# Performance work log

Hardware: AMD Instinct MI355X
Metric: run time of the kernel (lower is better)

Reference implementation:

```python
import math
import jax, jax.numpy as jnp
import numpy as np

HIDDEN = 2048
NUM_HEADS = 32
HEAD_DIM = HIDDEN // NUM_HEADS
NUM_BLOCKS = 4
INTER = 2 * HIDDEN
EPS = 1e-5
ROPE_THETA = 10000.0


def setup_inputs() -> dict:
    key = jax.random.key(0)
    ks = jax.random.split(key, 6)
    B, S = 2, 2048
    sc = 0.02
    return {
        "x": jax.random.normal(ks[0], (B, S, HIDDEN), jnp.float32),
        "attn_norm_w": jnp.ones((HIDDEN,), jnp.float32),
        "ffn_norm_w": jnp.ones((HIDDEN,), jnp.float32),
        "w_qkv": jax.random.normal(ks[1], (3 * HIDDEN, HIDDEN), jnp.float32) * sc,
        "w_o": jax.random.normal(ks[2], (HIDDEN, HIDDEN), jnp.float32) * sc,
        "w_up": jax.random.normal(ks[3], (2 * INTER, HIDDEN), jnp.float32) * sc,
        "w_down": jax.random.normal(ks[4], (HIDDEN, INTER), jnp.float32) * sc,
    }


def _rmsnorm(x, w):
    var = jnp.mean(x * x, axis=-1, keepdims=True)
    return x * jax.lax.rsqrt(var + EPS) * w


def _rope_cache(seq_len, dim, theta, scale):
    inv_freq = 1.0 / (theta ** (jnp.arange(0, dim, 2, dtype=jnp.float32) / dim))
    t = jnp.arange(seq_len, dtype=jnp.float32) / scale
    freqs = jnp.outer(t, inv_freq)                     # [S, D/2]
    emb = jnp.concatenate([freqs, freqs], axis=-1)     # [S, D]
    return jnp.cos(emb), jnp.sin(emb)


def _apply_rope(x, cos, sin):
    # x: [B, H, S, D]
    d2 = x.shape[-1] // 2
    x1, x2 = x[..., :d2], x[..., d2:]
    rot = jnp.concatenate([-x2, x1], axis=-1)
    return x * cos[None, None] + rot * sin[None, None]


def reference(x, attn_norm_w, ffn_norm_w, w_qkv, w_o, w_up, w_down):
    B, S, _ = x.shape
    residual = x
    h = _rmsnorm(x, attn_norm_w)

    qkv = jnp.einsum('bsh,oh->bso', h, w_qkv)
    qkv = qkv.reshape(B, S, 3, NUM_HEADS, HEAD_DIM)
    q, k, v = qkv[:, :, 0], qkv[:, :, 1], qkv[:, :, 2]
    q = q.transpose(0, 2, 1, 3)  # [B,H,S,D]
    k = k.transpose(0, 2, 1, 3)
    v = v.transpose(0, 2, 1, 3)

    cos, sin = _rope_cache(S, HEAD_DIM, ROPE_THETA, 1.0)
    q = _apply_rope(q, cos, sin)
    k = _apply_rope(k, cos, sin)

    scale = 1.0 / math.sqrt(HEAD_DIM)
    attn = jnp.einsum('bhqd,bhkd->bhqk', q, k) * scale

    num_blocks = max(1, min(NUM_BLOCKS, S))
    blk = math.ceil(S / num_blocks)
    pos = jnp.arange(S)
    block_ids = pos // blk
    block_mask = block_ids[:, None] != block_ids[None, :]
    causal_mask = pos[:, None] < pos[None, :]
    invalid = causal_mask | block_mask                 # [S,S]
    mask_floor = jnp.finfo(attn.dtype).min
    attn = jnp.where(invalid[None, None], mask_floor, attn)

    attn = jax.nn.softmax(attn, axis=-1)
    context = jnp.einsum('bhqk,bhkd->bhqd', attn, v)
    context = context.transpose(0, 2, 1, 3).reshape(B, S, HIDDEN)

    x = residual + jnp.einsum('bsh,oh->bso', context, w_o)

    residual = x
    h = _rmsnorm(x, ffn_norm_w)
    up = jnp.einsum('bsh,oh->bso', h, w_up)
    gate, value = up[..., :INTER], up[..., INTER:]
    down = jnp.einsum('bsi,oi->bso', jax.nn.silu(gate) * value, w_down)
    return residual + down
```

## Files before the change

kernel.cpp:

```cpp
#include <hip/hip_runtime.h>
#include <cstdint>
#include <cstddef>

typedef __bf16 bf16x8 __attribute__((ext_vector_type(8)));
typedef __bf16 bf16x4 __attribute__((ext_vector_type(4)));
typedef float  f32x4  __attribute__((ext_vector_type(4)));

#define TOKENS  4096
#define SEQLEN  2048
#define HID     2048
#define QKV_W   6144
#define UP_W    8192
#define INTER_  4096

__device__ __forceinline__ void async16(const void* g, void* l) {
  __builtin_amdgcn_global_load_lds(
      (__attribute__((address_space(1))) void*)(g),
      (__attribute__((address_space(3))) void*)(l), 16, 0, 0);
}

__global__ __launch_bounds__(256) void cvt_kernel(const float* __restrict__ src,
                                                  __bf16* __restrict__ dst, int n4) {
  int i = blockIdx.x * 256 + threadIdx.x;
  if (i >= n4) return;
  float4 f = ((const float4*)src)[i];
  bf16x4 o;
  o[0] = (__bf16)f.x; o[1] = (__bf16)f.y; o[2] = (__bf16)f.z; o[3] = (__bf16)f.w;
  ((bf16x4*)dst)[i] = o;
}

__global__ __launch_bounds__(256) void rmsnorm_kernel(const float* __restrict__ x,
                                                      const float* __restrict__ wgt,
                                                      __bf16* __restrict__ out) {
  const int tok = blockIdx.x;
  const int t = threadIdx.x;
  const float4* xr = (const float4*)(x + (long)tok * HID);
  float4 a = xr[t], b = xr[t + 256];
  float ss = a.x*a.x + a.y*a.y + a.z*a.z + a.w*a.w
           + b.x*b.x + b.y*b.y + b.z*b.z + b.w*b.w;
  #pragma unroll
  for (int off = 32; off; off >>= 1) ss += __shfl_xor(ss, off);
  __shared__ float red[4];
  if ((t & 63) == 0) red[t >> 6] = ss;
  __syncthreads();
  float tot = red[0] + red[1] + red[2] + red[3];
  float r = rsqrtf(tot * (1.0f / HID) + 1e-5f);
  const float4* wr = (const float4*)wgt;
  float4 wa = wr[t], wb = wr[t + 256];
  bf16x4 o0, o1;
  o0[0] = (__bf16)(a.x * r * wa.x); o0[1] = (__bf16)(a.y * r * wa.y);
  o0[2] = (__bf16)(a.z * r * wa.z); o0[3] = (__bf16)(a.w * r * wa.w);
  o1[0] = (__bf16)(b.x * r * wb.x); o1[1] = (__bf16)(b.y * r * wb.y);
  o1[2] = (__bf16)(b.z * r * wb.z); o1[3] = (__bf16)(b.w * r * wb.w);
  bf16x4* orow = (bf16x4*)(out + (long)tok * HID);
  orow[t] = o0; orow[t + 256] = o1;
}

template<bool OUT_BF16, bool ADD_RES, bool ROPE, bool SILU>
__global__ __launch_bounds__(256) void gemm_bt(const __bf16* __restrict__ A, int lda,
                                               const __bf16* __restrict__ B, int ldb,
                                               void* Cv, int ldc,
                                               const float* __restrict__ Res, int K) {
  __shared__ __align__(16) __bf16 As[128 * 64];
  __shared__ __align__(16) __bf16 Bs[128 * 64];
  const int t = threadIdx.x;
  const int lane = t & 63;
  const int w = t >> 6;
  const int wm = (w >> 1) * 64, wn = (w & 1) * 64;
  const int m0 = blockIdx.y * 128;
  const int n0 = SILU ? blockIdx.x * 64 : blockIdx.x * 128;
  const int sr = t >> 3;
  const int sc = (((t & 7) ^ (sr & 7)) * 8);
  const __bf16* Ag = A + (long)(m0 + sr) * lda + sc;
  const __bf16* Bg = B + (long)(n0 + sr) * ldb + sc;
  char* lA = (char*)As + t * 16;
  char* lB = (char*)Bs + t * 16;
  const int lr = lane & 15;
  const int lq = lane >> 4;
  f32x4 acc[4][4] = {};
  for (int k0 = 0; k0 < K; k0 += 64) {
    __syncthreads();
    #pragma unroll
    for (int c = 0; c < 4; c++)
      async16(Ag + (long)(c * 32) * lda + k0, lA + c * 4096);
    #pragma unroll
    for (int c = 0; c < 4; c++) {
      const long rowoff = SILU ? (long)((c & 1) * INTER_ + (c >> 1) * 32) * ldb
                               : (long)(c * 32) * ldb;
      async16(Bg + rowoff + k0, lB + c * 4096);
    }
    __syncthreads();
    #pragma unroll
    for (int ks = 0; ks < 2; ks++) {
      const int pos = (((ks * 4 + lq) ^ (lr & 7)) * 8);
      bf16x8 af[4], bfr[4];
      #pragma unroll
      for (int i = 0; i < 4; i++)
        af[i]  = *(const bf16x8*)(As + (wm + i * 16 + lr) * 64 + pos);
      #pragma unroll
      for (int j = 0; j < 4; j++)
        bfr[j] = *(const bf16x8*)(Bs + (wn + j * 16 + lr) * 64 + pos);
      #pragma unroll
      for (int i = 0; i < 4; i++)
        #pragma unroll
        for (int j = 0; j < 4; j++)
          acc[i][j] = __builtin_amdgcn_mfma_f32_16x16x32_bf16(af[i], bfr[j], acc[i][j], 0, 0, 0);
    }
  }
  const int lq4 = lq * 4;
  #pragma unroll
  for (int i = 0; i < 4; i++) {
    #pragma unroll
    for (int r = 0; r < 4; r++) {
      const long row = m0 + wm + i * 16 + lq4 + r;
      #pragma unroll
      for (int j = 0; j < 4; j++) {
        const long col = n0 + wn + j * 16 + lr;
        float v = acc[i][j][r];
        if (ADD_RES) v += Res[row * (long)ldc + col];
        if (OUT_BF16) ((__bf16*)Cv)[row * (long)ldc + col] = (__bf16)v;
        else          ((float*)Cv)[row * (long)ldc + col] = v;
      }
    }
  }
}

template<bool ROPE, bool SILU>
__global__ __launch_bounds__(512, 2) void gemm8p(const __bf16* __restrict__ A, int lda,
                                                 const __bf16* __restrict__ B, int ldb,
                                                 void* Cv, int ldc, int K) {
  __shared__ __align__(16) __bf16 As[2 * 16384];
  __shared__ __align__(16) __bf16 Bs[2 * 16384];
  const int tid  = threadIdx.x;
  const int lane = tid & 63;
  const int w    = tid >> 6;
  const int wm2  = w >> 2;
  const int wn4  = w & 3;
  const int lr   = lane & 15;
  const int lq   = lane >> 4;
  const int m0   = blockIdx.y * 256;
  const int n0   = ROPE ? blockIdx.x * 256 : 0;
  const int n0c  = SILU ? blockIdx.x * 128 : 0;

  const long r0 = tid >> 3;
  const int  e  = (((tid & 7) ^ ((int)r0 & 7)) * 8);
  const __bf16* Ap0 = A + (long)(m0 + r0) * lda + e;
  long br0, br1, bhs;
  if (ROPE) {
    br0 = n0 + 64 * (((int)r0 >> 5) & 3) + ((int)r0 & 31);
    br1 = n0 + 64 * ((((int)r0 + 64) >> 5) & 3) + ((int)r0 & 31);
    bhs = 32 * (long)ldb;
  } else {
    br0 = n0c + r0;
    br1 = n0c + r0 + 64;
    bhs = (long)INTER_ * ldb;
  }
  const __bf16* Bp0 = B + br0 * ldb + e;
  const __bf16* Bp1 = B + br1 * ldb + e;
  char* sA = (char*)As;
  char* sB = (char*)Bs;
  const int tid16 = tid * 16;

#define STAGE_A(h_, nb_, kk_) do {                                                     \
    async16(Ap0 + (long)((h_) * 128) * lda + (kk_),      sA + (nb_)*32768 + (h_)*16384 + tid16);        \
    async16(Ap0 + (long)((h_) * 128 + 64) * lda + (kk_), sA + (nb_)*32768 + (h_)*16384 + 8192 + tid16); \
  } while (0)
#define STAGE_B(h_, nb_, kk_) do {                                                     \
    async16(Bp0 + (h_) * bhs + (kk_), sB + (nb_)*32768 + (h_)*16384 + tid16);          \
    async16(Bp1 + (h_) * bhs + (kk_), sB + (nb_)*32768 + (h_)*16384 + 8192 + tid16);   \
  } while (0)

  const int ch0 = ((lq ^ (lr & 7)) * 16);
  const int ch1 = (((4 + lq) ^ (lr & 7)) * 16);
  const int abase = (wm2 * 64 + lr) * 128;
  const int bbase = (wn4 * 32 + lr) * 128;

  f32x4 acc[8][4] = {};
  bf16x8 af[4][2], bfr[4][2];
  const int NT = K >> 6;

#define LOAD_A(mh_) do {                                                               \
    _Pragma("unroll")                                                                  \
    for (int i = 0; i < 4; i++) {                                                      \
      af[i][0] = *(const bf16x8*)(Ab + abase + (mh_)*16384 + i*2048 + ch0);            \
      af[i][1] = *(const bf16x8*)(Ab + abase + (mh_)*16384 + i*2048 + ch1);            \
    } } while (0)
#define LOAD_B(nh_) do {                                                               \
    _Pragma("unroll")                                                                  \
    for (int j = 0; j < 2; j++) {                                                      \
      bfr[(nh_)*2 + j][0] = *(const bf16x8*)(Bb + bbase + (nh_)*16384 + j*2048 + ch0); \
      bfr[(nh_)*2 + j][1] = *(const bf16x8*)(Bb + bbase + (nh_)*16384 + j*2048 + ch1); \
    } } while (0)
#define MFMA_Q(mh_, nh_) do {                                                          \
    __builtin_amdgcn_s_setprio(1);                                                     \
    _Pragma("unroll")                                                                  \
    for (int ks = 0; ks < 2; ks++)                                                     \
      _Pragma("unroll")                                                                \
      for (int i = 0; i < 4; i++)                                                      \
        _Pragma("unroll")                                                              \
        for (int j = 0; j < 2; j++)                                                    \
          acc[(mh_)*4 + i][(nh_)*2 + j] = __builtin_amdgcn_mfma_f32_16x16x32_bf16(     \
              af[i][ks], bfr[(nh_)*2 + j][ks], acc[(mh_)*4 + i][(nh_)*2 + j], 0, 0, 0);\
    __builtin_amdgcn_s_setprio(0);                                                     \
  } while (0)
#define SBAR() do { __builtin_amdgcn_sched_barrier(0);                                 \
    __builtin_amdgcn_s_barrier(); __builtin_amdgcn_sched_barrier(0); } while (0)
#define LGKM0() do { asm volatile("s_waitcnt lgkmcnt(0)" ::: "memory");                \
    __builtin_amdgcn_sched_barrier(0); } while (0)

  STAGE_A(0, 0, 0); STAGE_B(0, 0, 0); STAGE_B(1, 0, 0); STAGE_A(1, 0, 0);
  asm volatile("s_waitcnt vmcnt(4)" ::: "memory");
  SBAR();

  for (int T = 0; T < NT; ++T) {
    const int cb = T & 1, nb = cb ^ 1;
    const int kk = (T + 1) << 6;
    const bool st = (T + 1 < NT);
    const char* Ab = (const char*)As + cb * 32768;
    const char* Bb = (const char*)Bs + cb * 32768;
    LOAD_A(0); LOAD_B(0);
    if (st) { STAGE_A(0, nb, kk); STAGE_B(0, nb, kk); }
    SBAR(); LGKM0();
    MFMA_Q(0, 0);
    if (st) asm volatile("s_waitcnt vmcnt(6)" ::: "memory");
    else    asm volatile("s_waitcnt vmcnt(2)" ::: "memory");
    SBAR();
    LOAD_B(1);
    if (st) STAGE_B(1, nb, kk);
    SBAR(); LGKM0();
    MFMA_Q(0, 1);
    if (st) asm volatile("s_waitcnt vmcnt(6)" ::: "memory");
    else    asm volatile("s_waitcnt vmcnt(0)" ::: "memory");
    SBAR();
    LOAD_A(1);
    if (st) STAGE_A(1, nb, kk);
    SBAR(); LGKM0();
    MFMA_Q(1, 0);
    SBAR();
    MFMA_Q(1, 1);
    if (st) asm volatile("s_waitcnt vmcnt(4)" ::: "memory");
    SBAR();
  }
#undef STAGE_A
#undef STAGE_B
#undef LOAD_A
#undef LOAD_B
#undef MFMA_Q
#undef SBAR
#undef LGKM0

  const int lq4 = lq * 4;
  if (ROPE) {
    if (n0 < 4096) {
      const float invf0 = exp2f((float)(lr)      * -0.41524101186092029f);
      const float invf1 = exp2f((float)(16 + lr) * -0.41524101186092029f);
      #pragma unroll
      for (int mi = 0; mi < 8; mi++) {
        #pragma unroll
        for (int r = 0; r < 4; r++) {
          const long row = m0 + (mi >> 2) * 128 + wm2 * 64 + (mi & 3) * 16 + lq4 + r;
          const float s = (float)(int)(row & (SEQLEN - 1));
          __bf16* crow = (__bf16*)Cv + row * (long)ldc + n0 + wn4 * 64 + lr;
          #pragma unroll
          for (int nj = 0; nj < 2; nj++) {
            float x1 = acc[mi][nj][r], x2 = acc[mi][nj + 2][r];
            float ang = s * (nj ? invf1 : invf0);
            float sn, cs;
            __sincosf(ang, &sn, &cs);
            crow[nj * 16]      = (__bf16)(x1 * cs - x2 * sn);
            crow[nj * 16 + 32] = (__bf16)(x2 * cs + x1 * sn);
          }
        }
      }
    } else {
      #pragma unroll
      for (int mi = 0; mi < 8; mi++) {
        #pragma unroll
        for (int r = 0; r < 4; r++) {
          const long row = m0 + (mi >> 2) * 128 + wm2 * 64 + (mi & 3) * 16 + lq4 + r;
          __bf16* crow = (__bf16*)Cv + row * (long)ldc + n0 + wn4 * 64 + lr;
          #pragma unroll
          for (int njf = 0; njf < 4; njf++)
            crow[(njf >> 1) * 32 + (njf & 1) * 16] = (__bf16)acc[mi][njf][r];
        }
      }
    }
  } else {
    #pragma unroll
    for (int mi = 0; mi < 8; mi++) {
      #pragma unroll
      for (int r = 0; r < 4; r++) {
        const long row = m0 + (mi >> 2) * 128 + wm2 * 64 + (mi & 3) * 16 + lq4 + r;
        #pragma unroll
        for (int nj = 0; nj < 2; nj++) {
          const long col = n0c + wn4 * 32 + nj * 16 + lr;
          float g = acc[mi][nj][r];
          float v = acc[mi][nj + 2][r];
          float sg = g / (1.0f + __expf(-g));
          ((__bf16*)Cv)[row * (long)ldc + col] = (__bf16)(sg * v);
        }
      }
    }
  }
}

__global__ __launch_bounds__(256) void attn_kernel(const __bf16* __restrict__ qkv,
                                                   __bf16* __restrict__ ctx) {
  const int qt   = blockIdx.x;
  const int head = blockIdx.y;
  const int b    = blockIdx.z;
  const int w    = threadIdx.x >> 6;
  const int lane = threadIdx.x & 63;
  const int lr = lane & 15;
  const int lq = lane >> 4;
  const int q0   = qt * 64;
  const int blk0 = q0 & ~511;
  const int nkv  = q0 + 64 - blk0;
  const int NT   = nkv >> 5;
  const long tok0 = (long)b * SEQLEN;

  const int qrow = q0 + w * 16 + lr;
  const long qoff = (tok0 + qrow) * QKV_W + head * 64 + lq * 8;
  bf16x8 qf0 = *(const bf16x8*)(qkv + qoff);
  bf16x8 qf1 = *(const bf16x8*)(qkv + qoff + 32);

  __shared__ __align__(16) char VTb[8192];
  __shared__ __align__(16) char Pbb[8192];

  const __bf16* kp = qkv + (tok0 + blk0 + lr) * QKV_W + HID + head * 64 + lq * 8;
  const int skv = threadIdx.x & 31;
  const int sd0 = (threadIdx.x >> 5) * 8;
  const __bf16* vp = qkv + (tok0 + blk0 + skv) * QKV_W + 2 * HID + head * 64 + sd0;

  bf16x8 ka[2][2], kb[2][2];

#define LOADK(KN, tk) do { \
    KN[0][0] = *(const bf16x8*)(kp + (long)(tk) * QKV_W); \
    KN[0][1] = *(const bf16x8*)(kp + (long)(tk) * QKV_W + 32); \
    KN[1][0] = *(const bf16x8*)(kp + (long)((tk) + 16) * QKV_W); \
    KN[1][1] = *(const bf16x8*)(kp + (long)((tk) + 16) * QKV_W + 32); \
  } while (0)

#define WRITEV(vr_, hb_) do { \
    const int c_ = (hb_) * 4 + (skv >> 3); \
    char* vb_ = VTb + sd0 * 128 + ((skv & 7) * 2); \
    _Pragma("unroll") \
    for (int i_ = 0; i_ < 8; i_++) \
      *(__bf16*)(vb_ + i_ * 128 + ((c_ ^ i_) * 16)) = vr_[i_]; \
  } while (0)

  LOADK(ka, 0);
  {
    bf16x8 vr0 = *(const bf16x8*)(vp);
    WRITEV(vr0, 0);
  }
  __syncthreads();

  float m[4], l[4];
  f32x4 oacc[4] = {};
  #pragma unroll
  for (int r = 0; r < 4; r++) { m[r] = -1e30f; l[r] = 0.0f; }
  const int myrow = q0 + w * 16 + lq * 4;

#define ITER(t_, hb_, KC, KN) { \
    const int tkn_ = ((t_) + 1) * 32; \
    const bool more_ = ((t_) + 1 < NT); \
    bf16x8 vr_ = {}; \
    if (more_) { LOADK(KN, tkn_); vr_ = *(const bf16x8*)(vp + (long)tkn_ * QKV_W); } \
    f32x4 s0 = {0.f, 0.f, 0.f, 0.f}, s1 = {0.f, 0.f, 0.f, 0.f}; \
    s0 = __builtin_amdgcn_mfma_f32_16x16x32_bf16(qf0, KC[0][0], s0, 0, 0, 0); \
    s0 = __builtin_amdgcn_mfma_f32_16x16x32_bf16(qf1, KC[0][1], s0, 0, 0, 0); \
    s1 = __builtin_amdgcn_mfma_f32_16x16x32_bf16(qf0, KC[1][0], s1, 0, 0, 0); \
    s1 = __builtin_amdgcn_mfma_f32_16x16x32_bf16(qf1, KC[1][1], s1, 0, 0, 0); \
    const int kpos0_ = blk0 + (t_) * 32 + lr; \
    float p0[4], p1[4], alpha[4]; \
    _Pragma("unroll") \
    for (int r = 0; r < 4; r++) { \
      float v0 = s0[r] * 0.125f, v1 = s1[r] * 0.125f; \
      v0 = (kpos0_      <= myrow + r) ? v0 : -1e30f; \
      v1 = (kpos0_ + 16 <= myrow + r) ? v1 : -1e30f; \
      float mx = fmaxf(v0, v1); \
      mx = fmaxf(mx, __shfl_xor(mx, 1)); \
      mx = fmaxf(mx, __shfl_xor(mx, 2)); \
      mx = fmaxf(mx, __shfl_xor(mx, 4)); \
      mx = fmaxf(mx, __shfl_xor(mx, 8)); \
      float mn = fmaxf(m[r], mx); \
      alpha[r] = __expf(m[r] - mn); \
      m[r] = mn; \
      p0[r] = __expf(v0 - mn); \
      p1[r] = __expf(v1 - mn); \
      float rs = p0[r] + p1[r]; \
      rs += __shfl_xor(rs, 1); rs += __shfl_xor(rs, 2); \
      rs += __shfl_xor(rs, 4); rs += __shfl_xor(rs, 8); \
      l[r] = l[r] * alpha[r] + rs; \
    } \
    _Pragma("unroll") \
    for (int dt = 0; dt < 4; dt++) \
      _Pragma("unroll") \
      for (int r = 0; r < 4; r++) oacc[dt][r] *= alpha[r]; \
    { \
      char* pw_ = Pbb + w * 2048 + (lq * 4) * 128 + ((lr & 7) * 2); \
      const int cl_ = (hb_) * 4 + (lr >> 3); \
      _Pragma("unroll") \
      for (int r = 0; r < 4; r++) { \
        const int q7_ = (lq * 4 + r) & 7; \
        *(__bf16*)(pw_ + r * 128 + (((cl_    ) ^ q7_) * 16)) = (__bf16)p0[r]; \
        *(__bf16*)(pw_ + r * 128 + (((cl_ + 2) ^ q7_) * 16)) = (__bf16)p1[r]; \
      } \
    } \
    asm volatile("s_waitcnt lgkmcnt(0)" ::: "memory"); \
    const int swz_ = (((hb_) * 4 + lq) ^ (lr & 7)) * 16; \
    bf16x8 pf_ = *(const bf16x8*)(Pbb + w * 2048 + lr * 128 + swz_); \
    _Pragma("unroll") \
    for (int dt = 0; dt < 4; dt++) { \
      bf16x8 vf_ = *(const bf16x8*)(VTb + dt * 2048 + lr * 128 + swz_); \
      oacc[dt] = __builtin_amdgcn_mfma_f32_16x16x32_bf16(pf_, vf_, oacc[dt], 0, 0, 0); \
    } \
    __syncthreads(); \
    if (more_) WRITEV(vr_, (hb_) ^ 1); \
    __syncthreads(); \
  }

  for (int t2 = 0; t2 < NT; t2 += 2) {
    ITER(t2, 0, ka, kb)
    ITER(t2 + 1, 1, kb, ka)
  }
#undef ITER
#undef LOADK
#undef WRITEV

  #pragma unroll
  for (int r = 0; r < 4; r++) {
    float inv = 1.0f / l[r];
    long obase = (tok0 + myrow + r) * HID + head * 64;
    #pragma unroll
    for (int dt = 0; dt < 4; dt++)
      ctx[obase + dt * 16 + lr] = (__bf16)(oacc[dt][r] * inv);
  }
}

extern "C" void kernel_launch(void* const* d_in, const int* in_sizes, int n_in,
                              void* d_out, int out_size, void* d_ws, size_t ws_size,
                              hipStream_t stream) {
  const float* x      = (const float*)d_in[0];
  const float* anw    = (const float*)d_in[1];
  const float* fnw    = (const float*)d_in[2];
  const float* w_qkv  = (const float*)d_in[3];
  const float* w_o    = (const float*)d_in[4];
  const float* w_up   = (const float*)d_in[5];
  const float* w_down = (const float*)d_in[6];
  float* out = (float*)d_out;

  char* wsb = (char*)d_ws;
  __bf16* ABUF = (__bf16*)wsb;
  __bf16* QKV  = (__bf16*)(wsb + (size_t)16777216);
  __bf16* WBUF = (__bf16*)(wsb + (size_t)83886080);
  __bf16* ACT  = QKV;

  rmsnorm_kernel<<<TOKENS, 256, 0, stream>>>(x, anw, ABUF);
  cvt_kernel<<<(QKV_W * HID / 4 + 255) / 256, 256, 0, stream>>>(w_qkv, WBUF, QKV_W * HID / 4);
  gemm8p<true, false><<<dim3(4096 / 256, TOKENS / 256), 512, 0, stream>>>(
      ABUF, HID, WBUF, HID, (void*)QKV, QKV_W, HID);
  gemm_bt<true, false, false, false><<<dim3(HID / 128, TOKENS / 128), 256, 0, stream>>>(
      ABUF, HID, WBUF + (size_t)4096 * HID, HID, (void*)(QKV + 4096), QKV_W, nullptr, HID);
  attn_kernel<<<dim3(SEQLEN / 64, 32, 2), 256, 0, stream>>>(QKV, ABUF);
  cvt_kernel<<<(HID * HID / 4 + 255) / 256, 256, 0, stream>>>(w_o, WBUF, HID * HID / 4);
  gemm_bt<false, true, false, false><<<dim3(HID / 128, TOKENS / 128), 256, 0, stream>>>(
      ABUF, HID, WBUF, HID, (void*)out, HID, x, HID);

  rmsnorm_kernel<<<TOKENS, 256, 0, stream>>>(out, fnw, ABUF);
  cvt_kernel<<<(UP_W * HID / 4 + 255) / 256, 256, 0, stream>>>(w_up, WBUF, UP_W * HID / 4);
  gemm8p<false, true><<<dim3(INTER_ / 128, TOKENS / 256), 512, 0, stream>>>(
      ABUF, HID, WBUF, HID, (void*)ACT, INTER_, HID);
  cvt_kernel<<<(HID * INTER_ / 4 + 255) / 256, 256, 0, stream>>>(w_down, WBUF, HID * INTER_ / 4);
  gemm_bt<false, true, false, false><<<dim3(HID / 128, TOKENS / 128), 256, 0, stream>>>(
      ACT, INTER_, WBUF, INTER_, (void*)out, HID, out, INTER_);
}
```

Baseline: 553.0 us.

## Add BK=32 specialized up-projection GEMM with SwiGLU epilogue and higher occupancy

Adds a dedicated kernel for the FFN up-projection that uses a K-tile of 32 with double-buffered async global-to-LDS loads. It also uses a swizzled LDS layout and a staged load/MFMA schedule with explicit waitcnts and barriers. The smaller LDS footprint and launch bounds of 4 blocks per CU aim to raise occupancy and overlap loads with MFMA work. In exchange it runs more loop iterations with more barriers per unit of K.

```diff
diff --git a/kernel.cpp b/kernel.cpp
--- a/kernel.cpp
+++ b/kernel.cpp
@@ -299,6 +299,124 @@
           float sg = g / (1.0f + __expf(-g));
           ((__bf16*)Cv)[row * (long)ldc + col] = (__bf16)(sg * v);
         }
+      }
+    }
+  }
+}
+
+__global__ __launch_bounds__(512, 4) void gemm_up32(const __bf16* __restrict__ A, int lda,
+                                                    const __bf16* __restrict__ B, int ldb,
+                                                    void* Cv, int ldc, int K) {
+  __shared__ __align__(16) __bf16 As[2 * 8192];
+  __shared__ __align__(16) __bf16 Bs[2 * 8192];
+  const int tid  = threadIdx.x;
+  const int lane = tid & 63;
+  const int w    = tid >> 6;
+  const int wm2  = w >> 2;
+  const int wn4  = w & 3;
+  const int lr   = lane & 15;
+  const int lq   = lane >> 4;
+  const int m0   = blockIdx.y * 256;
+  const int n0c  = blockIdx.x * 128;
+
+  const int sr = tid >> 2;
+  const int g8 = ((((tid & 3) - ((tid >> 3) & 3)) & 3) * 8);
+  const __bf16* ApS = A + (long)(m0 + sr) * lda + g8;
+  const __bf16* BpS = B + (long)(n0c + sr) * ldb + g8;
+  char* sA = (char*)As;
+  char* sB = (char*)Bs;
+  const int tid16 = tid * 16;
+
+#define STAGE_A32(h_, nb_, kk_) \
+    async16(ApS + (long)((h_) * 128) * lda + (kk_), sA + (nb_)*16384 + (h_)*8192 + tid16)
+#define STAGE_B32(h_, nb_, kk_) \
+    async16(BpS + (h_) * ((long)INTER_ * ldb) + (kk_), sB + (nb_)*16384 + (h_)*8192 + tid16)
+
+  const int p16   = ((lq + ((lr >> 1) & 3)) & 3) * 16;
+  const int abase = (wm2 * 64 + lr) * 64 + p16;
+  const int bbase = (wn4 * 32 + lr) * 64 + p16;
+
+  f32x4 acc[8][4] = {};
+  bf16x8 af[4], bfr[4];
+  const int NT = K >> 5;
+
+#define LOAD_A32(mh_, buf_) do {                                                       \
+    const char* p_ = sA + (buf_)*16384 + (mh_)*8192 + abase;                           \
+    _Pragma("unroll")                                                                  \
+    for (int i = 0; i < 4; i++) af[i] = *(const bf16x8*)(p_ + i * 1024);               \
+  } while (0)
+#define LOAD_B32(nh_, buf_) do {                                                       \
+    const char* p_ = sB + (buf_)*16384 + (nh_)*8192 + bbase;                           \
+    _Pragma("unroll")                                                                  \
+    for (int j = 0; j < 2; j++) bfr[(nh_)*2 + j] = *(const bf16x8*)(p_ + j * 1024);    \
+  } while (0)
+#define MFMA_Q32(mh_, nh_) do {                                                        \
+    __builtin_amdgcn_s_setprio(1);                                                     \
+    _Pragma("unroll")                                                                  \
+    for (int i = 0; i < 4; i++)                                                        \
+      _Pragma("unroll")                                                                \
+      for (int j = 0; j < 2; j++)                                                      \
+        acc[(mh_)*4 + i][(nh_)*2 + j] = __builtin_amdgcn_mfma_f32_16x16x32_bf16(       \
+            af[i], bfr[(nh_)*2 + j], acc[(mh_)*4 + i][(nh_)*2 + j], 0, 0, 0);          \
+    __builtin_amdgcn_s_setprio(0);                                                     \
+  } while (0)
+#define SBAR() do { __builtin_amdgcn_sched_barrier(0);                                 \
+    __builtin_amdgcn_s_barrier(); __builtin_amdgcn_sched_barrier(0); } while (0)
+#define LGKM0() do { asm volatile("s_waitcnt lgkmcnt(0)" ::: "memory");                \
+    __builtin_amdgcn_sched_barrier(0); } while (0)
+
+  STAGE_A32(0, 0, 0); STAGE_B32(0, 0, 0); STAGE_B32(1, 0, 0); STAGE_A32(1, 0, 0);
+  asm volatile("s_waitcnt vmcnt(1)" ::: "memory");
+  SBAR();
+
+  for (int T = 0; T < NT; ++T) {
+    const int cb = T & 1, nb = cb ^ 1;
+    const int kk = (T + 1) << 5;
+    const bool st = (T + 1 < NT);
+    LOAD_A32(0, cb); LOAD_B32(0, cb);
+    if (st) { STAGE_A32(0, nb, kk); STAGE_B32(0, nb, kk); }
+    SBAR(); LGKM0();
+    MFMA_Q32(0, 0);
+    if (st) asm volatile("s_waitcnt vmcnt(3)" ::: "memory");
+    else    asm volatile("s_waitcnt vmcnt(1)" ::: "memory");
+    SBAR();
+    LOAD_B32(1, cb);
+    if (st) STAGE_B32(1, nb, kk);
+    SBAR(); LGKM0();
+    MFMA_Q32(0, 1);
+    if (st) asm volatile("s_waitcnt vmcnt(3)" ::: "memory");
+    else    asm volatile("s_waitcnt vmcnt(0)" ::: "memory");
+    SBAR();
+    LOAD_A32(1, cb);
+    if (st) STAGE_A32(1, nb, kk);
+    SBAR(); LGKM0();
+    MFMA_Q32(1, 0);
+    SBAR();
+    MFMA_Q32(1, 1);
+    if (st) asm volatile("s_waitcnt vmcnt(2)" ::: "memory");
+    SBAR();
+  }
+#undef STAGE_A32
+#undef STAGE_B32
+#undef LOAD_A32
+#undef LOAD_B32
+#undef MFMA_Q32
+#undef SBAR
+#undef LGKM0
+
+  const int lq4 = lq * 4;
+  #pragma unroll
+  for (int mi = 0; mi < 8; mi++) {
+    #pragma unroll
+    for (int r = 0; r < 4; r++) {
+      const long row = m0 + (mi >> 2) * 128 + wm2 * 64 + (mi & 3) * 16 + lq4 + r;
+      #pragma unroll
+      for (int nj = 0; nj < 2; nj++) {
+        const long col = n0c + wn4 * 32 + nj * 16 + lr;
+        float g = acc[mi][nj][r];
+        float v = acc[mi][nj + 2][r];
+        float sg = g / (1.0f + __expf(-g));
+        ((__bf16*)Cv)[row * (long)ldc + col] = (__bf16)(sg * v);
       }
     }
   }
@@ -470,7 +588,7 @@
 
   rmsnorm_kernel<<<TOKENS, 256, 0, stream>>>(out, fnw, ABUF);
   cvt_kernel<<<(UP_W * HID / 4 + 255) / 256, 256, 0, stream>>>(w_up, WBUF, UP_W * HID / 4);
-  gemm8p<false, true><<<dim3(INTER_ / 128, TOKENS / 256), 512, 0, stream>>>(
+  gemm_up32<<<dim3(INTER_ / 128, TOKENS / 256), 512, 0, stream>>>(
       ABUF, HID, WBUF, HID, (void*)ACT, INTER_, HID);
   cvt_kernel<<<(HID * INTER_ / 4 + 255) / 256, 256, 0, stream>>>(w_down, WBUF, HID * INTER_ / 4);
   gemm_bt<false, true, false, false><<<dim3(HID / 128, TOKENS / 128), 256, 0, stream>>>(
```

Result: slower. 1.441 ms (+160.7%).

## Replace single-buffered GEMM with double-buffered 4-wave pipelined GEMM kernel

Applied to the files above, without the earlier changes.

Removes the simple gemm_bt kernel and adds gemm4w, a 128x128 tile GEMM with double-buffered LDS. It issues async global-to-LDS loads for the next K tile while the current one runs MFMAs, using explicit vmcnt/lgkmcnt waits, sched barriers and setprio. The aim is to hide global memory latency, which the old kernel exposed by waiting on loads before every K step. The SiLU up-projection also moves from the 8-wave 256-row gemm8p to this kernel with smaller tiles. That trades per-block reuse for more blocks and possibly higher occupancy.

```diff
diff --git a/kernel.cpp b/kernel.cpp
--- a/kernel.cpp
+++ b/kernel.cpp
@@ -54,75 +54,6 @@
   o1[2] = (__bf16)(b.z * r * wb.z); o1[3] = (__bf16)(b.w * r * wb.w);
   bf16x4* orow = (bf16x4*)(out + (long)tok * HID);
   orow[t] = o0; orow[t + 256] = o1;
-}
-
-template<bool OUT_BF16, bool ADD_RES, bool ROPE, bool SILU>
-__global__ __launch_bounds__(256) void gemm_bt(const __bf16* __restrict__ A, int lda,
-                                               const __bf16* __restrict__ B, int ldb,
-                                               void* Cv, int ldc,
-                                               const float* __restrict__ Res, int K) {
-  __shared__ __align__(16) __bf16 As[128 * 64];
-  __shared__ __align__(16) __bf16 Bs[128 * 64];
-  const int t = threadIdx.x;
-  const int lane = t & 63;
-  const int w = t >> 6;
-  const int wm = (w >> 1) * 64, wn = (w & 1) * 64;
-  const int m0 = blockIdx.y * 128;
-  const int n0 = SILU ? blockIdx.x * 64 : blockIdx.x * 128;
-  const int sr = t >> 3;
-  const int sc = (((t & 7) ^ (sr & 7)) * 8);
-  const __bf16* Ag = A + (long)(m0 + sr) * lda + sc;
-  const __bf16* Bg = B + (long)(n0 + sr) * ldb + sc;
-  char* lA = (char*)As + t * 16;
-  char* lB = (char*)Bs + t * 16;
-  const int lr = lane & 15;
-  const int lq = lane >> 4;
-  f32x4 acc[4][4] = {};
-  for (int k0 = 0; k0 < K; k0 += 64) {
-    __syncthreads();
-    #pragma unroll
-    for (int c = 0; c < 4; c++)
-      async16(Ag + (long)(c * 32) * lda + k0, lA + c * 4096);
-    #pragma unroll
-    for (int c = 0; c < 4; c++) {
-      const long rowoff = SILU ? (long)((c & 1) * INTER_ + (c >> 1) * 32) * ldb
-                               : (long)(c * 32) * ldb;
-      async16(Bg + rowoff + k0, lB + c * 4096);
-    }
-    __syncthreads();
-    #pragma unroll
-    for (int ks = 0; ks < 2; ks++) {
-      const int pos = (((ks * 4 + lq) ^ (lr & 7)) * 8);
-      bf16x8 af[4], bfr[4];
-      #pragma unroll
-      for (int i = 0; i < 4; i++)
-        af[i]  = *(const bf16x8*)(As + (wm + i * 16 + lr) * 64 + pos);
-      #pragma unroll
-      for (int j = 0; j < 4; j++)
-        bfr[j] = *(const bf16x8*)(Bs + (wn + j * 16 + lr) * 64 + pos);
-      #pragma unroll
-      for (int i = 0; i < 4; i++)
-        #pragma unroll
-        for (int j = 0; j < 4; j++)
-          acc[i][j] = __builtin_amdgcn_mfma_f32_16x16x32_bf16(af[i], bfr[j], acc[i][j], 0, 0, 0);
-    }
-  }
-  const int lq4 = lq * 4;
-  #pragma unroll
-  for (int i = 0; i < 4; i++) {
-    #pragma unroll
-    for (int r = 0; r < 4; r++) {
-      const long row = m0 + wm + i * 16 + lq4 + r;
-      #pragma unroll
-      for (int j = 0; j < 4; j++) {
-        const long col = n0 + wn + j * 16 + lr;
-        float v = acc[i][j][r];
-        if (ADD_RES) v += Res[row * (long)ldc + col];
-        if (OUT_BF16) ((__bf16*)Cv)[row * (long)ldc + col] = (__bf16)v;
-        else          ((float*)Cv)[row * (long)ldc + col] = v;
-      }
-    }
-  }
 }
 
 template<bool ROPE, bool SILU>
@@ -298,6 +229,159 @@
           float v = acc[mi][nj + 2][r];
           float sg = g / (1.0f + __expf(-g));
           ((__bf16*)Cv)[row * (long)ldc + col] = (__bf16)(sg * v);
+        }
+      }
+    }
+  }
+}
+
+template<bool OUT_BF16, bool ADD_RES, bool SILU>
+__global__ __launch_bounds__(256, 2) void gemm4w(const __bf16* __restrict__ A, int lda,
+                                                 const __bf16* __restrict__ B, int ldb,
+                                                 void* Cv, int ldc,
+                                                 const float* __restrict__ Res, int K) {
+  __shared__ __align__(16) __bf16 As[2 * 8192];
+  __shared__ __align__(16) __bf16 Bs[2 * 8192];
+  const int tid  = threadIdx.x;
+  const int lane = tid & 63;
+  const int w    = tid >> 6;
+  const int wm1  = w >> 1;
+  const int wn1  = w & 1;
+  const int lr   = lane & 15;
+  const int lq   = lane >> 4;
+  const int m0   = blockIdx.y * 128;
+  const int n0   = SILU ? 0 : blockIdx.x * 128;
+  const int n0c  = SILU ? blockIdx.x * 64 : 0;
+
+  const int r0 = tid >> 3;
+  const int e  = (((tid & 7) ^ (r0 & 7)) * 8);
+  const __bf16* ApS = A + (long)(m0 + r0) * lda + e;
+  long br0, bhs;
+  if (SILU) { br0 = n0c + r0; bhs = (long)INTER_ * ldb; }
+  else      { br0 = n0 + r0;  bhs = 64 * (long)ldb; }
+  const __bf16* BpS = B + br0 * ldb + e;
+  char* sA = (char*)As;
+  char* sB = (char*)Bs;
+  const int tid16 = tid * 16;
+
+#define STAGE_A(h_, nb_, kk_) do {                                                       \
+    async16(ApS + (long)((h_) * 64) * lda + (kk_),      sA + (nb_)*16384 + (h_)*8192 + tid16);        \
+    async16(ApS + (long)((h_) * 64 + 32) * lda + (kk_), sA + (nb_)*16384 + (h_)*8192 + 4096 + tid16); \
+  } while (0)
+#define STAGE_B(h_, nb_, kk_) do {                                                       \
+    async16(BpS + (h_) * bhs + (kk_),                   sB + (nb_)*16384 + (h_)*8192 + tid16);        \
+    async16(BpS + (h_) * bhs + 32 * (long)ldb + (kk_),  sB + (nb_)*16384 + (h_)*8192 + 4096 + tid16); \
+  } while (0)
+
+  const int ch0 = ((lq ^ (lr & 7)) * 16);
+  const int ch1 = (((4 + lq) ^ (lr & 7)) * 16);
+  const int abase = (wm1 * 32 + lr) * 128;
+  const int bbase = (wn1 * 32 + lr) * 128;
+
+  f32x4 acc[4][4] = {};
+  bf16x8 af[2][2], bfr[4][2];
+  const int NT = K >> 6;
+
+#define LOAD_A(mh_) do {                                                                 \
+    _Pragma("unroll")                                                                    \
+    for (int i = 0; i < 2; i++) {                                                        \
+      af[i][0] = *(const bf16x8*)(Ab + abase + (mh_)*8192 + i*2048 + ch0);               \
+      af[i][1] = *(const bf16x8*)(Ab + abase + (mh_)*8192 + i*2048 + ch1);               \
+    } } while (0)
+#define LOAD_B(nh_) do {                                                                 \
+    _Pragma("unroll")                                                                    \
+    for (int j = 0; j < 2; j++) {                                                        \
+      bfr[(nh_)*2 + j][0] = *(const bf16x8*)(Bb + bbase + (nh_)*8192 + j*2048 + ch0);    \
+      bfr[(nh_)*2 + j][1] = *(const bf16x8*)(Bb + bbase + (nh_)*8192 + j*2048 + ch1);    \
+    } } while (0)
+#define MFMA_Q(mh_, nh_) do {                                                            \
+    __builtin_amdgcn_s_setprio(1);                                                       \
+    _Pragma("unroll")                                                                    \
+    for (int ks = 0; ks < 2; ks++)                                                       \
+      _Pragma("unroll")                                                                  \
+      for (int i = 0; i < 2; i++)                                                        \
+        _Pragma("unroll")                                                                \
+        for (int j = 0; j < 2; j++)                                                      \
+          acc[(mh_)*2 + i][(nh_)*2 + j] = __builtin_amdgcn_mfma_f32_16x16x32_bf16(       \
+              af[i][ks], bfr[(nh_)*2 + j][ks], acc[(mh_)*2 + i][(nh_)*2 + j], 0, 0, 0);  \
+    __builtin_amdgcn_s_setprio(0);                                                       \
+  } while (0)
+#define SBAR() do { __builtin_amdgcn_sched_barrier(0);                                   \
+    __builtin_amdgcn_s_barrier(); __builtin_amdgcn_sched_barrier(0); } while (0)
+#define LGKM0() do { asm volatile("s_waitcnt lgkmcnt(0)" ::: "memory");                  \
+    __builtin_amdgcn_sched_barrier(0); } while (0)
+
+  STAGE_A(0, 0, 0); STAGE_B(0, 0, 0); STAGE_B(1, 0, 0); STAGE_A(1, 0, 0);
+  asm volatile("s_waitcnt vmcnt(4)" ::: "memory");
+  SBAR();
+
+  for (int T = 0; T < NT; ++T) {
+    const int cb = T & 1, nb = cb ^ 1;
+    const int kk = (T + 1) << 6;
+    const bool st = (T + 1 < NT);
+    const char* Ab = (const char*)As + cb * 16384;
+    const char* Bb = (const char*)Bs + cb * 16384;
+    LOAD_A(0); LOAD_B(0);
+    if (st) { STAGE_A(0, nb, kk); STAGE_B(0, nb, kk); }
+    SBAR(); LGKM0();
+    MFMA_Q(0, 0);
+    if (st) asm volatile("s_waitcnt vmcnt(6)" ::: "memory");
+    else    asm volatile("s_waitcnt vmcnt(2)" ::: "memory");
+    SBAR();
+    LOAD_B(1);
+    if (st) STAGE_B(1, nb, kk);
+    SBAR(); LGKM0();
+    MFMA_Q(0, 1);
+    if (st) asm volatile("s_waitcnt vmcnt(6)" ::: "memory");
+    else    asm volatile("s_waitcnt vmcnt(0)" ::: "memory");
+    SBAR();
+    LOAD_A(1);
+    if (st) STAGE_A(1, nb, kk);
+    SBAR(); LGKM0();
+    MFMA_Q(1, 0);
+    SBAR();
+    MFMA_Q(1, 1);
+    if (st) asm volatile("s_waitcnt vmcnt(4)" ::: "memory");
+    SBAR();
+  }
+#undef STAGE_A
+#undef STAGE_B
+#undef LOAD_A
+#undef LOAD_B
+#undef MFMA_Q
+#undef SBAR
+#undef LGKM0
+
+  const int lq4 = lq * 4;
+  if (SILU) {
+    #pragma unroll
+    for (int mi = 0; mi < 4; mi++) {
+      #pragma unroll
+      for (int r = 0; r < 4; r++) {
+        const long row = m0 + (mi >> 1) * 64 + wm1 * 32 + (mi & 1) * 16 + lq4 + r;
+        #pragma unroll
+        for (int nj = 0; nj < 2; nj++) {
+          const long col = n0c + wn1 * 32 + nj * 16 + lr;
+          float g = acc[mi][nj][r];
+          float v = acc[mi][nj + 2][r];
+          float sg = g / (1.0f + __expf(-g));
+          ((__bf16*)Cv)[row * (long)ldc + col] = (__bf16)(sg * v);
+        }
+      }
+    }
+  } else {
+    #pragma unroll
+    for (int mi = 0; mi < 4; mi++) {
+      #pragma unroll
+      for (int r = 0; r < 4; r++) {
+        const long row = m0 + (mi >> 1) * 64 + wm1 * 32 + (mi & 1) * 16 + lq4 + r;
+        #pragma unroll
+        for (int nj = 0; nj < 4; nj++) {
+          const long col = n0 + (nj >> 1) * 64 + wn1 * 32 + (nj & 1) * 16 + lr;
+          float v = acc[mi][nj][r];
+          if (ADD_RES) v += Res[row * (long)ldc + col];
+          if (OUT_BF16) ((__bf16*)Cv)[row * (long)ldc + col] = (__bf16)v;
+          else          ((float*)Cv)[row * (long)ldc + col] = v;
         }
       }
     }
@@ -461,18 +545,18 @@
   cvt_kernel<<<(QKV_W * HID / 4 + 255) / 256, 256, 0, stream>>>(w_qkv, WBUF, QKV_W * HID / 4);
   gemm8p<true, false><<<dim3(4096 / 256, TOKENS / 256), 512, 0, stream>>>(
       ABUF, HID, WBUF, HID, (void*)QKV, QKV_W, HID);
-  gemm_bt<true, false, false, false><<<dim3(HID / 128, TOKENS / 128), 256, 0, stream>>>(
+  gemm4w<true, false, false><<<dim3(HID / 128, TOKENS / 128), 256, 0, stream>>>(
       ABUF, HID, WBUF + (size_t)4096 * HID, HID, (void*)(QKV + 4096), QKV_W, nullptr, HID);
   attn_kernel<<<dim3(SEQLEN / 64, 32, 2), 256, 0, stream>>>(QKV, ABUF);
   cvt_kernel<<<(HID * HID / 4 + 255) / 256, 256, 0, stream>>>(w_o, WBUF, HID * HID / 4);
-  gemm_bt<false, true, false, false><<<dim3(HID / 128, TOKENS / 128), 256, 0, stream>>>(
+  gemm4w<false, true, false><<<dim3(HID / 128, TOKENS / 128), 256, 0, stream>>>(
       ABUF, HID, WBUF, HID, (void*)out, HID, x, HID);
 
   rmsnorm_kernel<<<TOKENS, 256, 0, stream>>>(out, fnw, ABUF);
   cvt_kernel<<<(UP_W * HID / 4 + 255) / 256, 256, 0, stream>>>(w_up, WBUF, UP_W * HID / 4);
-  gemm8p<false, true><<<dim3(INTER_ / 128, TOKENS / 256), 512, 0, stream>>>(
-      ABUF, HID, WBUF, HID, (void*)ACT, INTER_, HID);
+  gemm4w<true, false, true><<<dim3(INTER_ / 64, TOKENS / 128), 256, 0, stream>>>(
+      ABUF, HID, WBUF, HID, (void*)ACT, INTER_, nullptr, HID);
   cvt_kernel<<<(HID * INTER_ / 4 + 255) / 256, 256, 0, stream>>>(w_down, WBUF, HID * INTER_ / 4);
-  gemm_bt<false, true, false, false><<<dim3(HID / 128, TOKENS / 128), 256, 0, stream>>>(
+  gemm4w<false, true, false><<<dim3(HID / 128, TOKENS / 128), 256, 0, stream>>>(
       ACT, INTER_, WBUF, INTER_, (void*)out, HID, out, INTER_);
 }
```

Result: no change. 563.4 us (+1.9%).

## Widen attention KV tile to 64 keys and double-buffer V in LDS

Applied to the files above, without the earlier changes.

The block-causal attention kernel now processes 64 keys per iteration instead of 32. It issues four QK MFMA tiles per step and two PV k-slices. V is double-buffered in shared memory, so each iteration needs one barrier instead of two. This cuts loop trip count, barrier and softmax-reduction overhead per key. In exchange it raises register pressure, because K prefetch registers double, and uses more LDS, which may reduce occupancy.

```diff
diff --git a/kernel.cpp b/kernel.cpp
--- a/kernel.cpp
+++ b/kernel.cpp
@@ -316,7 +316,7 @@
   const int q0   = qt * 64;
   const int blk0 = q0 & ~511;
   const int nkv  = q0 + 64 - blk0;
-  const int NT   = nkv >> 5;
+  const int NT   = nkv >> 6;
   const long tok0 = (long)b * SEQLEN;
 
   const int qrow = q0 + w * 16 + lr;
@@ -324,35 +324,37 @@
   bf16x8 qf0 = *(const bf16x8*)(qkv + qoff);
   bf16x8 qf1 = *(const bf16x8*)(qkv + qoff + 32);
 
-  __shared__ __align__(16) char VTb[8192];
+  __shared__ __align__(16) char VTb[2][8192];
   __shared__ __align__(16) char Pbb[8192];
 
+  const int skv = threadIdx.x & 63;
+  const int sd0 = (threadIdx.x >> 6) * 8;
+  const __bf16* vp = qkv + (tok0 + blk0 + skv) * QKV_W + 2 * HID + head * 64 + sd0;
   const __bf16* kp = qkv + (tok0 + blk0 + lr) * QKV_W + HID + head * 64 + lq * 8;
-  const int skv = threadIdx.x & 31;
-  const int sd0 = (threadIdx.x >> 5) * 8;
-  const __bf16* vp = qkv + (tok0 + blk0 + skv) * QKV_W + 2 * HID + head * 64 + sd0;
-
-  bf16x8 ka[2][2], kb[2][2];
-
-#define LOADK(KN, tk) do { \
-    KN[0][0] = *(const bf16x8*)(kp + (long)(tk) * QKV_W); \
-    KN[0][1] = *(const bf16x8*)(kp + (long)(tk) * QKV_W + 32); \
-    KN[1][0] = *(const bf16x8*)(kp + (long)((tk) + 16) * QKV_W); \
-    KN[1][1] = *(const bf16x8*)(kp + (long)((tk) + 16) * QKV_W + 32); \
-  } while (0)
-
-#define WRITEV(vr_, hb_) do { \
-    const int c_ = (hb_) * 4 + (skv >> 3); \
-    char* vb_ = VTb + sd0 * 128 + ((skv & 7) * 2); \
-    _Pragma("unroll") \
-    for (int i_ = 0; i_ < 8; i_++) \
-      *(__bf16*)(vb_ + i_ * 128 + ((c_ ^ i_) * 16)) = vr_[i_]; \
-  } while (0)
+
+#define WRITEV(va_, vb_, bf_) do { \
+    const int c_ = skv >> 3; \
+    char* p_ = VTb[bf_] + sd0 * 128 + ((skv & 7) * 2); \
+    _Pragma("unroll") \
+    for (int i_ = 0; i_ < 8; i_++) { \
+      *(__bf16*)(p_ + i_ * 128 + ((c_ ^ i_) * 16))        = va_[i_]; \
+      *(__bf16*)(p_ + (32 + i_) * 128 + ((c_ ^ i_) * 16)) = vb_[i_]; \
+    } } while (0)
+
+#define LOADK(KN_, tk_) do { \
+    _Pragma("unroll") \
+    for (int nt_ = 0; nt_ < 4; nt_++) { \
+      KN_[nt_][0] = *(const bf16x8*)(kp + (long)((tk_) + nt_ * 16) * QKV_W); \
+      KN_[nt_][1] = *(const bf16x8*)(kp + (long)((tk_) + nt_ * 16) * QKV_W + 32); \
+    } } while (0)
+
+  bf16x8 ka[4][2], kb[4][2];
 
   LOADK(ka, 0);
   {
-    bf16x8 vr0 = *(const bf16x8*)(vp);
-    WRITEV(vr0, 0);
+    bf16x8 va0 = *(const bf16x8*)(vp);
+    bf16x8 vb0 = *(const bf16x8*)(vp + 32);
+    WRITEV(va0, vb0, 0);
   }
   __syncthreads();
 
@@ -362,24 +364,33 @@
   for (int r = 0; r < 4; r++) { m[r] = -1e30f; l[r] = 0.0f; }
   const int myrow = q0 + w * 16 + lq * 4;
 
-#define ITER(t_, hb_, KC, KN) { \
-    const int tkn_ = ((t_) + 1) * 32; \
+#define ITER(t_, KC_, KN_) { \
+    const int bf_ = (t_) & 1; \
     const bool more_ = ((t_) + 1 < NT); \
-    bf16x8 vr_ = {}; \
-    if (more_) { LOADK(KN, tkn_); vr_ = *(const bf16x8*)(vp + (long)tkn_ * QKV_W); } \
-    f32x4 s0 = {0.f, 0.f, 0.f, 0.f}, s1 = {0.f, 0.f, 0.f, 0.f}; \
-    s0 = __builtin_amdgcn_mfma_f32_16x16x32_bf16(qf0, KC[0][0], s0, 0, 0, 0); \
-    s0 = __builtin_amdgcn_mfma_f32_16x16x32_bf16(qf1, KC[0][1], s0, 0, 0, 0); \
-    s1 = __builtin_amdgcn_mfma_f32_16x16x32_bf16(qf0, KC[1][0], s1, 0, 0, 0); \
-    s1 = __builtin_amdgcn_mfma_f32_16x16x32_bf16(qf1, KC[1][1], s1, 0, 0, 0); \
-    const int kpos0_ = blk0 + (t_) * 32 + lr; \
-    float p0[4], p1[4], alpha[4]; \
+    bf16x8 va_ = {}, vb_ = {}; \
+    if (more_) { \
+      const __bf16* vq_ = vp + (long)(((t_) + 1) * 64) * QKV_W; \
+      va_ = *(const bf16x8*)(vq_); \
+      vb_ = *(const bf16x8*)(vq_ + 32); \
+      LOADK(KN_, ((t_) + 1) * 64); \
+    } \
+    f32x4 s[4]; \
+    _Pragma("unroll") \
+    for (int nt = 0; nt < 4; nt++) { \
+      f32x4 z = {0.f, 0.f, 0.f, 0.f}; \
+      z = __builtin_amdgcn_mfma_f32_16x16x32_bf16(qf0, KC_[nt][0], z, 0, 0, 0); \
+      z = __builtin_amdgcn_mfma_f32_16x16x32_bf16(qf1, KC_[nt][1], z, 0, 0, 0); \
+      s[nt] = z; \
+    } \
+    const int kb0_ = blk0 + (t_) * 64 + lr; \
+    float p[4][4], alpha[4]; \
     _Pragma("unroll") \
     for (int r = 0; r < 4; r++) { \
-      float v0 = s0[r] * 0.125f, v1 = s1[r] * 0.125f; \
-      v0 = (kpos0_      <= myrow + r) ? v0 : -1e30f; \
-      v1 = (kpos0_ + 16 <= myrow + r) ? v1 : -1e30f; \
-      float mx = fmaxf(v0, v1); \
+      float v0 = (kb0_      <= myrow + r) ? s[0][r] * 0.125f : -1e30f; \
+      float v1 = (kb0_ + 16 <= myrow + r) ? s[1][r] * 0.125f : -1e30f; \
+      float v2 = (kb0_ + 32 <= myrow + r) ? s[2][r] * 0.125f : -1e30f; \
+      float v3 = (kb0_ + 48 <= myrow + r) ? s[3][r] * 0.125f : -1e30f; \
+      float mx = fmaxf(fmaxf(v0, v1), fmaxf(v2, v3)); \
       mx = fmaxf(mx, __shfl_xor(mx, 1)); \
       mx = fmaxf(mx, __shfl_xor(mx, 2)); \
       mx = fmaxf(mx, __shfl_xor(mx, 4)); \
@@ -387,11 +398,15 @@
       float mn = fmaxf(m[r], mx); \
       alpha[r] = __expf(m[r] - mn); \
       m[r] = mn; \
-      p0[r] = __expf(v0 - mn); \
-      p1[r] = __expf(v1 - mn); \
-      float rs = p0[r] + p1[r]; \
-      rs += __shfl_xor(rs, 1); rs += __shfl_xor(rs, 2); \
-      rs += __shfl_xor(rs, 4); rs += __shfl_xor(rs, 8); \
+      p[0][r] = __expf(v0 - mn); \
+      p[1][r] = __expf(v1 - mn); \
+      p[2][r] = __expf(v2 - mn); \
+      p[3][r] = __expf(v3 - mn); \
+      float rs = (p[0][r] + p[1][r]) + (p[2][r] + p[3][r]); \
+      rs += __shfl_xor(rs, 1); \
+      rs += __shfl_xor(rs, 2); \
+      rs += __shfl_xor(rs, 4); \
+      rs += __shfl_xor(rs, 8); \
       l[r] = l[r] * alpha[r] + rs; \
     } \
     _Pragma("unroll") \
@@ -399,31 +414,36 @@
       _Pragma("unroll") \
       for (int r = 0; r < 4; r++) oacc[dt][r] *= alpha[r]; \
     { \
-      char* pw_ = Pbb + w * 2048 + (lq * 4) * 128 + ((lr & 7) * 2); \
-      const int cl_ = (hb_) * 4 + (lr >> 3); \
+      char* pw = Pbb + w * 2048 + (lq * 4) * 128 + ((lr & 7) * 2); \
+      const int cb_ = lr >> 3; \
       _Pragma("unroll") \
       for (int r = 0; r < 4; r++) { \
-        const int q7_ = (lq * 4 + r) & 7; \
-        *(__bf16*)(pw_ + r * 128 + (((cl_    ) ^ q7_) * 16)) = (__bf16)p0[r]; \
-        *(__bf16*)(pw_ + r * 128 + (((cl_ + 2) ^ q7_) * 16)) = (__bf16)p1[r]; \
+        const int q7 = (lq * 4 + r) & 7; \
+        _Pragma("unroll") \
+        for (int nt = 0; nt < 4; nt++) \
+          *(__bf16*)(pw + r * 128 + (((nt * 2 + cb_) ^ q7) * 16)) = (__bf16)p[nt][r]; \
       } \
     } \
     asm volatile("s_waitcnt lgkmcnt(0)" ::: "memory"); \
-    const int swz_ = (((hb_) * 4 + lq) ^ (lr & 7)) * 16; \
-    bf16x8 pf_ = *(const bf16x8*)(Pbb + w * 2048 + lr * 128 + swz_); \
-    _Pragma("unroll") \
-    for (int dt = 0; dt < 4; dt++) { \
-      bf16x8 vf_ = *(const bf16x8*)(VTb + dt * 2048 + lr * 128 + swz_); \
-      oacc[dt] = __builtin_amdgcn_mfma_f32_16x16x32_bf16(pf_, vf_, oacc[dt], 0, 0, 0); \
-    } \
-    __syncthreads(); \
-    if (more_) WRITEV(vr_, (hb_) ^ 1); \
-    __syncthreads(); \
+    _Pragma("unroll") \
+    for (int h = 0; h < 2; h++) { \
+      const int swz = (((h * 4 + lq) ^ (lr & 7)) * 16); \
+      bf16x8 pf = *(const bf16x8*)(Pbb + w * 2048 + lr * 128 + swz); \
+      _Pragma("unroll") \
+      for (int dt = 0; dt < 4; dt++) { \
+        bf16x8 vf = *(const bf16x8*)(VTb[bf_] + (dt * 16 + lr) * 128 + swz); \
+        oacc[dt] = __builtin_amdgcn_mfma_f32_16x16x32_bf16(pf, vf, oacc[dt], 0, 0, 0); \
+      } \
+    } \
+    if (more_) { \
+      WRITEV(va_, vb_, bf_ ^ 1); \
+      __syncthreads(); \
+    } \
   }
 
   for (int t2 = 0; t2 < NT; t2 += 2) {
-    ITER(t2, 0, ka, kb)
-    ITER(t2 + 1, 1, kb, ka)
+    ITER(t2, ka, kb)
+    if (t2 + 1 < NT) ITER(t2 + 1, kb, ka)
   }
 #undef ITER
 #undef LOADK
```

Result: no change. 560.7 us (+1.4%).
